# Optimization experiments

Hardware: AMD Instinct MI355X
Metric: run time of the kernel (lower is better)

The kernel has to match this reference:

```python
import jax, jax.numpy as jnp
import numpy as np
from jax import lax

B, S, D, H, T = 128, 512, 128, 128, 20


def setup_inputs() -> dict:
    key = jax.random.key(0)
    ks = jax.random.split(key, 16)
    sc = 1.0 / np.sqrt(H)
    u = lambda k, shape: jax.random.uniform(k, shape, jnp.float32, -sc, sc)
    return {
        "inputs": jax.random.normal(ks[0], (B, S, D), jnp.float32),
        "tags": jax.random.randint(ks[1], (B, S), 0, T),
        "mask": jnp.ones((B, S), jnp.bool_),
        "w_ih_f": u(ks[2], (4 * H, D)),
        "w_hh_f": u(ks[3], (4 * H, H)),
        "b_f": u(ks[4], (4 * H,)),
        "w_ih_b": u(ks[5], (4 * H, D)),
        "w_hh_b": u(ks[6], (4 * H, H)),
        "b_b": u(ks[7], (4 * H,)),
        "w_out": u(ks[8], (T, 2 * H)),
        "b_out": u(ks[9], (T,)),
        "start_trans": jax.random.uniform(ks[10], (T,), jnp.float32, -0.1, 0.1),
        "end_trans": jax.random.uniform(ks[11], (T,), jnp.float32, -0.1, 0.1),
        "trans": jax.random.uniform(ks[12], (T, T), jnp.float32, -0.1, 0.1),
    }


def _lstm_dir(x, w_ih, w_hh, b, reverse):
    # x: [B,S,D] -> hidden states [B,S,H]
    xp = jnp.einsum('bsd,gd->bsg', x, w_ih) + b  # precomputed input gates [B,S,4H]
    if reverse:
        xp = xp[:, ::-1]
    h0 = jnp.zeros((x.shape[0], H), x.dtype)
    c0 = jnp.zeros((x.shape[0], H), x.dtype)

    def step(carry, xt):
        h, c = carry
        g = xt + h @ w_hh.T
        i, f, gg, o = jnp.split(g, 4, axis=-1)
        i, f, o = jax.nn.sigmoid(i), jax.nn.sigmoid(f), jax.nn.sigmoid(o)
        c = f * c + i * jnp.tanh(gg)
        h = o * jnp.tanh(c)
        return (h, c), h

    _, hs = lax.scan(step, (h0, c0), xp.transpose(1, 0, 2))
    hs = hs.transpose(1, 0, 2)  # [B,S,H]
    if reverse:
        hs = hs[:, ::-1]
    return hs


def _crf_nll(em, tags, mask, start_trans, end_trans, trans):
    # em: [B,S,T]; torchcrf log-likelihood, reduction='mean', negated
    b, s, t = em.shape
    maskf = mask.astype(em.dtype)
    batch = jnp.arange(b)
    # numerator: score of the gold path
    num = start_trans[tags[:, 0]] + em[batch, 0, tags[:, 0]]
    em_tag = jnp.take_along_axis(em, tags[:, :, None], axis=2)[:, :, 0]  # [B,S]
    trans_tag = trans[tags[:, :-1], tags[:, 1:]]  # [B,S-1]
    num = num + jnp.sum((trans_tag + em_tag[:, 1:]) * maskf[:, 1:], axis=1)
    seq_ends = jnp.sum(mask.astype(jnp.int32), axis=1) - 1
    num = num + end_trans[tags[batch, seq_ends]]
    # denominator: forward algorithm (logsumexp semiring) via scan
    score0 = start_trans[None, :] + em[:, 0]  # [B,T]

    def step(score, inp):
        em_t, m_t = inp
        nxt = jax.nn.logsumexp(score[:, :, None] + trans[None] + em_t[:, None, :], axis=1)
        return jnp.where(m_t[:, None], nxt, score), None

    score, _ = lax.scan(step, score0, (em[:, 1:].transpose(1, 0, 2), mask[:, 1:].T))
    den = jax.nn.logsumexp(score + end_trans[None, :], axis=1)
    return -jnp.mean(num - den)


def reference(inputs, tags, mask, w_ih_f, w_hh_f, b_f, w_ih_b, w_hh_b, b_b,
              w_out, b_out, start_trans, end_trans, trans):
    h_f = _lstm_dir(inputs, w_ih_f, w_hh_f, b_f, reverse=False)
    h_b = _lstm_dir(inputs, w_ih_b, w_hh_b, b_b, reverse=True)
    lstm_out = jnp.concatenate([h_f, h_b], axis=-1)  # [B,S,2H]
    emissions = jnp.einsum('bsh,th->bst', lstm_out, w_out) + b_out  # [B,S,T]
    return _crf_nll(emissions, tags, mask, start_trans, end_trans, trans)
```

## Files before the change

### kernel.cpp

```cpp
#include <hip/hip_runtime.h>
#include <cstdint>
#include <cstddef>

#define DEVINL __device__ __forceinline__

constexpr int Bz = 128, Sl = 512, Dm = 128, Hd = 128, NC = 1024, Tt = 20;
constexpr int Mrows = Bz * Sl;

constexpr size_t OFF_WBF  = 0;
constexpr size_t OFF_HS   = 151261184;
constexpr size_t OFF_EM   = 184815616;
constexpr size_t OFF_PART = 190058496;

constexpr float LOG2E  = 1.4426950408889634f;
constexpr float LOG2E2 = 2.8853900817779268f;

DEVINL unsigned short f2bf(float f) {
    uint32_t u = __float_as_uint(f);
    u += 0x7fffu + ((u >> 16) & 1u);
    return (unsigned short)(u >> 16);
}
DEVINL float bf2f(unsigned short h) { return __uint_as_float(((uint32_t)h) << 16); }

DEVINL float rcpf(float x) { return __builtin_amdgcn_rcpf(x); }
DEVINL float exp2f_fast(float x) { return __builtin_amdgcn_exp2f(x); }

DEVINL void barrier_lds_only() {
    __asm__ __volatile__("s_waitcnt lgkmcnt(0)" ::: "memory");
    __builtin_amdgcn_s_barrier();
    __asm__ __volatile__("" ::: "memory");
}

typedef __attribute__((ext_vector_type(8))) __bf16 bf16x8;
typedef __attribute__((ext_vector_type(4))) float f32x4;
typedef _Float16 __attribute__((ext_vector_type(2))) half2_t;
typedef _Float16 __attribute__((ext_vector_type(8))) half8_t;

__global__ __launch_bounds__(256) void wcvt_k(
    const float* __restrict__ wf, const float* __restrict__ wb,
    unsigned short* __restrict__ o)
{
    const int idx = (blockIdx.x * 256 + threadIdx.x) * 4;
    const float* src = (idx < 65536) ? (wf + idx) : (wb + (idx - 65536));
    float4 v = *(const float4*)src;
    ushort4 u; u.x = f2bf(v.x); u.y = f2bf(v.y); u.z = f2bf(v.z); u.w = f2bf(v.w);
    *(ushort4*)(o + idx) = u;
}

__global__ __launch_bounds__(512, 1) void lstm_k(
    const float* __restrict__ X, const unsigned short* __restrict__ wbf,
    const float* __restrict__ b_f, const float* __restrict__ b_b,
    const float* __restrict__ whf, const float* __restrict__ whb,
    unsigned short* __restrict__ hs)
{
    __shared__ __align__(16) unsigned short xl[512 * 72];
    __shared__ __align__(16) unsigned short Xs[64 * 132];
    __shared__ __align__(16) _Float16 h_buf[2][128];
    const int dir = blockIdx.x >> 7;
    const int b   = blockIdx.x & 127;
    const int tid = threadIdx.x;
    const int lane = tid & 63;
    const int wv   = tid >> 6;
    const int ln   = lane & 15;
    const int qd   = lane >> 4;
    const int u    = wv * 16 + ln;

    const float* wsrc = dir ? whb : whf;
    half8_t wfr[4][4];
    #pragma unroll
    for (int j = 0; j < 4; ++j) {
        const float sc = (j == 2) ? LOG2E2 : LOG2E;
        const float* wrow = wsrc + (size_t)(j * 128 + u) * 128;
        #pragma unroll
        for (int kk = 0; kk < 4; ++kk) {
            float4 v0 = *(const float4*)(wrow + kk * 32 + qd * 8);
            float4 v1 = *(const float4*)(wrow + kk * 32 + qd * 8 + 4);
            half8_t hv;
            hv[0] = (_Float16)(v0.x * sc); hv[1] = (_Float16)(v0.y * sc);
            hv[2] = (_Float16)(v0.z * sc); hv[3] = (_Float16)(v0.w * sc);
            hv[4] = (_Float16)(v1.x * sc); hv[5] = (_Float16)(v1.y * sc);
            hv[6] = (_Float16)(v1.z * sc); hv[7] = (_Float16)(v1.w * sc);
            wfr[j][kk] = hv;
        }
    }

    bf16x8 wih[4][4];
    #pragma unroll
    for (int n = 0; n < 4; ++n)
        #pragma unroll
        for (int k = 0; k < 4; ++k)
            wih[n][k] = *(const bf16x8*)&wbf[((size_t)(dir * 512 + wv * 64 + n * 16 + ln)) * 128
                                            + k * 32 + qd * 8];
    const float* bsrc = dir ? b_b : b_f;
    float bvn[4];
    #pragma unroll
    for (int n = 0; n < 4; ++n) bvn[n] = bsrc[wv * 64 + n * 16 + ln];
    const float scw = ((wv >> 1) == 2) ? LOG2E2 : LOG2E;

    if (tid < 128) { h_buf[0][tid] = (_Float16)0.f; h_buf[1][tid] = (_Float16)0.f; }
    __syncthreads();

    const float* Xb = X + (size_t)b * 512 * 128;
    const int colc = (tid & 31) * 4, rowb = tid >> 5;

    unsigned short* hptr = hs + (size_t)dir * Mrows * 128 + (size_t)b * Sl * 128 + u
                              + (dir ? (size_t)(Sl - 1) * 128 : 0);
    const int hstep = dir ? -128 : 128;

    float c = 0.f;
    const f32x4 zc = {0.f, 0.f, 0.f, 0.f};

    const int r0 = (0 * 128 + u) * 72;
    const int r1 = (1 * 128 + u) * 72;
    const int r2 = (2 * 128 + u) * 72;
    const int r3 = (3 * 128 + u) * 72;

    for (int ch = 0; ch < 8; ++ch) {
        const int tlo = dir ? (448 - 64 * ch) : (64 * ch);

        #pragma unroll
        for (int r = 0; r < 4; ++r) {
            const int row = rowb + r * 16;
            float4 av = *(const float4*)&Xb[(size_t)(tlo + row) * 128 + colc];
            ushort4 au; au.x = f2bf(av.x); au.y = f2bf(av.y); au.z = f2bf(av.z); au.w = f2bf(av.w);
            *(ushort4*)&Xs[row * 132 + colc] = au;
        }
        barrier_lds_only();

        {
            f32x4 acc[4][4];
            #pragma unroll
            for (int k = 0; k < 4; ++k) {
                const int kb = k * 32 + qd * 8;
                bf16x8 af[4];
                #pragma unroll
                for (int m = 0; m < 4; ++m)
                    af[m] = *(const bf16x8*)&Xs[(m * 16 + ln) * 132 + kb];
                #pragma unroll
                for (int m = 0; m < 4; ++m)
                    #pragma unroll
                    for (int n = 0; n < 4; ++n)
                        acc[m][n] = (k == 0)
                            ? __builtin_amdgcn_mfma_f32_16x16x32_bf16(af[m], wih[n][0], zc, 0, 0, 0)
                            : __builtin_amdgcn_mfma_f32_16x16x32_bf16(af[m], wih[n][k], acc[m][n], 0, 0, 0);
            }
            #pragma unroll
            for (int m = 0; m < 4; ++m)
                #pragma unroll
                for (int n = 0; n < 4; ++n) {
                    const int gg = wv * 64 + n * 16 + ln;
                    ushort4 o;
                    o.x = f2bf((acc[m][n][0] + bvn[n]) * scw);
                    o.y = f2bf((acc[m][n][1] + bvn[n]) * scw);
                    o.z = f2bf((acc[m][n][2] + bvn[n]) * scw);
                    o.w = f2bf((acc[m][n][3] + bvn[n]) * scw);
                    *(ushort4*)&xl[gg * 72 + m * 16 + qd * 4] = o;
                }
        }
        barrier_lds_only();

        const int tt0 = dir ? 60 : 0;
        ushort4 cur0, cur1, cur2, cur3;
        {
            ushort4 q0 = *(const ushort4*)&xl[r0 + tt0];
            ushort4 q1 = *(const ushort4*)&xl[r1 + tt0];
            ushort4 q2 = *(const ushort4*)&xl[r2 + tt0];
            ushort4 q3 = *(const ushort4*)&xl[r3 + tt0];
            cur0 = dir ? ushort4{q0.w, q0.z, q0.y, q0.x} : q0;
            cur1 = dir ? ushort4{q1.w, q1.z, q1.y, q1.x} : q1;
            cur2 = dir ? ushort4{q2.w, q2.z, q2.y, q2.x} : q2;
            cur3 = dir ? ushort4{q3.w, q3.z, q3.y, q3.x} : q3;
        }

        for (int gi = 0; gi < 16; ++gi) {
            #pragma unroll
            for (int j = 0; j < 4; ++j) {
                __asm__ __volatile__(""
                    : "+v"(wfr[j][0]), "+v"(wfr[j][1]), "+v"(wfr[j][2]), "+v"(wfr[j][3]));
            }
            int ttn = dir ? (56 - gi * 4) : (gi * 4 + 4);
            if (ttn < 0) ttn = 0;
            ushort4 n0 = *(const ushort4*)&xl[r0 + ttn];
            ushort4 n1 = *(const ushort4*)&xl[r1 + ttn];
            ushort4 n2 = *(const ushort4*)&xl[r2 + ttn];
            ushort4 n3 = *(const ushort4*)&xl[r3 + ttn];

            #pragma unroll
            for (int s = 0; s < 4; ++s) {
                const int p = s & 1;
                const half8_t* hb = (const half8_t*)&h_buf[p][0];
                half8_t a0 = hb[qd];
                half8_t a1 = hb[4 + qd];
                half8_t a2 = hb[8 + qd];
                half8_t a3 = hb[12 + qd];

                f32x4 ac0, ac1, ac2, ac3;
                ac0 = __builtin_amdgcn_mfma_f32_16x16x32_f16(a0, wfr[0][0], zc, 0, 0, 0);
                ac1 = __builtin_amdgcn_mfma_f32_16x16x32_f16(a0, wfr[1][0], zc, 0, 0, 0);
                ac2 = __builtin_amdgcn_mfma_f32_16x16x32_f16(a0, wfr[2][0], zc, 0, 0, 0);
                ac3 = __builtin_amdgcn_mfma_f32_16x16x32_f16(a0, wfr[3][0], zc, 0, 0, 0);
                ac0 = __builtin_amdgcn_mfma_f32_16x16x32_f16(a1, wfr[0][1], ac0, 0, 0, 0);
                ac1 = __builtin_amdgcn_mfma_f32_16x16x32_f16(a1, wfr[1][1], ac1, 0, 0, 0);
                ac2 = __builtin_amdgcn_mfma_f32_16x16x32_f16(a1, wfr[2][1], ac2, 0, 0, 0);
                ac3 = __builtin_amdgcn_mfma_f32_16x16x32_f16(a1, wfr[3][1], ac3, 0, 0, 0);
                ac0 = __builtin_amdgcn_mfma_f32_16x16x32_f16(a2, wfr[0][2], ac0, 0, 0, 0);
                ac1 = __builtin_amdgcn_mfma_f32_16x16x32_f16(a2, wfr[1][2], ac1, 0, 0, 0);
                ac2 = __builtin_amdgcn_mfma_f32_16x16x32_f16(a2, wfr[2][2], ac2, 0, 0, 0);
                ac3 = __builtin_amdgcn_mfma_f32_16x16x32_f16(a2, wfr[3][2], ac3, 0, 0, 0);
                ac0 = __builtin_amdgcn_mfma_f32_16x16x32_f16(a3, wfr[0][3], ac0, 0, 0, 0);
                ac1 = __builtin_amdgcn_mfma_f32_16x16x32_f16(a3, wfr[1][3], ac1, 0, 0, 0);
                ac2 = __builtin_amdgcn_mfma_f32_16x16x32_f16(a3, wfr[2][3], ac2, 0, 0, 0);
                ac3 = __builtin_amdgcn_mfma_f32_16x16x32_f16(a3, wfr[3][3], ac3, 0, 0, 0);

                const unsigned short xb0 = (s == 0) ? cur0.x : (s == 1) ? cur0.y : (s == 2) ? cur0.z : cur0.w;
                const unsigned short xb1 = (s == 0) ? cur1.x : (s == 1) ? cur1.y : (s == 2) ? cur1.z : cur1.w;
                const unsigned short xb2 = (s == 0) ? cur2.x : (s == 1) ? cur2.y : (s == 2) ? cur2.z : cur2.w;
                const unsigned short xb3 = (s == 0) ? cur3.x : (s == 1) ? cur3.y : (s == 2) ? cur3.z : cur3.w;

                float t0 = ac0[0] + bf2f(xb0);
                float t1 = ac1[0] + bf2f(xb1);
                float t2 = ac2[0] + bf2f(xb2);
                float t3 = ac3[0] + bf2f(xb3);

                float gi_ = rcpf(1.f + exp2f_fast(-t0));
                float gf_ = rcpf(1.f + exp2f_fast(-t1));
                float gg_ = 2.f * rcpf(1.f + exp2f_fast(-t2)) - 1.f;
                float go_ = rcpf(1.f + exp2f_fast(-t3));
                c = fmaf(gf_, c, gi_ * gg_);
                float th = 1.f - 2.f * rcpf(1.f + exp2f_fast(LOG2E2 * c));
                float h = go_ * th;

                if (qd == 0) {
                    _Float16 hh = (_Float16)h;
                    h_buf[1 - p][u] = hh;
                    unsigned short hbits; __builtin_memcpy(&hbits, &hh, 2);
                    *hptr = hbits;
                }
                hptr += hstep;
                barrier_lds_only();
            }
            cur0 = dir ? ushort4{n0.w, n0.z, n0.y, n0.x} : n0;
            cur1 = dir ? ushort4{n1.w, n1.z, n1.y, n1.x} : n1;
            cur2 = dir ? ushort4{n2.w, n2.z, n2.y, n2.x} : n2;
            cur3 = dir ? ushort4{n3.w, n3.z, n3.y, n3.x} : n3;
        }
    }
}

__global__ __launch_bounds__(320, 1) void emis_k(
    const unsigned short* __restrict__ hs, const float* __restrict__ wout,
    const float* __restrict__ bout, float* __restrict__ em)
{
    __shared__ __align__(16) half2_t wlds[20 * 128];
    const int b  = blockIdx.x >> 2;
    const int qt = blockIdx.x & 3;
    const int tid = threadIdx.x;

    #pragma unroll
    for (int k = 0; k < 8; ++k) {
        int i = tid + k * 320;
        wlds[i] = half2_t{(_Float16)wout[2 * i], (_Float16)wout[2 * i + 1]};
    }
    __syncthreads();

    const int tag  = tid % 20;
    const int copy = tid / 20;
    half2_t wreg[128];
    {
        const uint4* wl4 = (const uint4*)&wlds[tag * 128];
        #pragma unroll
        for (int k = 0; k < 32; ++k) {
            uint4 v = wl4[k];
            __builtin_memcpy(&wreg[4 * k], &v, 16);
        }
    }
    const float bo = bout[tag];
    const unsigned short* hf_base = hs + (size_t)b * Sl * 128;
    const unsigned short* hb_base = hs + (size_t)Mrows * 128 + (size_t)b * Sl * 128;

    #pragma unroll
    for (int i = 0; i < 8; ++i) {
        const int t = qt * 128 + copy + 16 * i;
        const uint4* hf4 = (const uint4*)(hf_base + (size_t)t * 128);
        const uint4* hb4 = (const uint4*)(hb_base + (size_t)t * 128);
        float a0 = bo, a1 = 0.f, a2 = 0.f, a3 = 0.f;
        #pragma unroll
        for (int k = 0; k < 16; ++k) {
            uint4 v = hf4[k];
            half2_t h2[4]; __builtin_memcpy(h2, &v, 16);
            a0 = __builtin_amdgcn_fdot2(wreg[4 * k + 0], h2[0], a0, false);
            a1 = __builtin_amdgcn_fdot2(wreg[4 * k + 1], h2[1], a1, false);
            a2 = __builtin_amdgcn_fdot2(wreg[4 * k + 2], h2[2], a2, false);
            a3 = __builtin_amdgcn_fdot2(wreg[4 * k + 3], h2[3], a3, false);
        }
        #pragma unroll
        for (int k = 0; k < 16; ++k) {
            uint4 v = hb4[k];
            half2_t h2[4]; __builtin_memcpy(h2, &v, 16);
            a0 = __builtin_amdgcn_fdot2(wreg[64 + 4 * k + 0], h2[0], a0, false);
            a1 = __builtin_amdgcn_fdot2(wreg[64 + 4 * k + 1], h2[1], a1, false);
            a2 = __builtin_amdgcn_fdot2(wreg[64 + 4 * k + 2], h2[2], a2, false);
            a3 = __builtin_amdgcn_fdot2(wreg[64 + 4 * k + 3], h2[3], a3, false);
        }
        em[((size_t)b * Sl + t) * Tt + tag] = (a0 + a1) + (a2 + a3);
    }
}

__global__ __launch_bounds__(64) void crf_k(
    const float* __restrict__ em, const int* __restrict__ tags,
    const float* __restrict__ st, const float* __restrict__ et,
    const float* __restrict__ trans, float* __restrict__ part)
{
    const int b = blockIdx.x, lane = threadIdx.x;
    const float* emb = em + (size_t)b * Sl * Tt;
    const int* tg = tags + (size_t)b * Sl;

    float nacc = 0.f;
    for (int t = 1 + lane; t < Sl; t += 64) {
        int tp = tg[t - 1], tc = tg[t];
        nacc += trans[tp * Tt + tc] + emb[t * Tt + tc];
    }
    #pragma unroll
    for (int off = 32; off; off >>= 1) nacc += __shfl_down(nacc, off);

    float Etr[20];
    #pragma unroll
    for (int i = 0; i < 20; ++i)
        Etr[i] = (lane < 20) ? __expf(trans[i * Tt + lane]) : 0.f;

    float C = 0.f;
    float p = (lane < 20) ? __expf(st[lane] + emb[lane]) : 0.f;

    float evr[8];
    #pragma unroll
    for (int s = 0; s < 8; ++s) {
        int tt = 1 + s; tt = tt < Sl ? tt : Sl - 1;
        evr[s] = (lane < 20) ? emb[(size_t)tt * Tt + lane] : 0.f;
    }

    for (int t0 = 1; t0 < Sl; t0 += 8) {
        #pragma unroll
        for (int s = 0; s < 8; ++s) {
            const int t = t0 + s;
            if (t < Sl) {
                float ev = evr[s];
                int tf = t + 8; tf = tf < Sl ? tf : Sl - 1;
                evr[s] = (lane < 20) ? emb[(size_t)tf * Tt + lane] : 0.f;

                float q0 = 0.f, q1 = 0.f, q2 = 0.f, q3 = 0.f;
                #pragma unroll
                for (int i = 0; i < 20; i += 4) {
                    q0 = fmaf(__int_as_float(__builtin_amdgcn_readlane(__float_as_int(p), i + 0)), Etr[i + 0], q0);
                    q1 = fmaf(__int_as_float(__builtin_amdgcn_readlane(__float_as_int(p), i + 1)), Etr[i + 1], q1);
                    q2 = fmaf(__int_as_float(__builtin_amdgcn_readlane(__float_as_int(p), i + 2)), Etr[i + 2], q2);
                    q3 = fmaf(__int_as_float(__builtin_amdgcn_readlane(__float_as_int(p), i + 3)), Etr[i + 3], q3);
                }
                p = ((q0 + q1) + (q2 + q3)) * __expf(ev);
                if ((s & 3) == 3) {
                    float S0 = 0.f, S1 = 0.f, S2 = 0.f, S3 = 0.f;
                    #pragma unroll
                    for (int i = 0; i < 20; i += 4) {
                        S0 += __int_as_float(__builtin_amdgcn_readlane(__float_as_int(p), i + 0));
                        S1 += __int_as_float(__builtin_amdgcn_readlane(__float_as_int(p), i + 1));
                        S2 += __int_as_float(__builtin_amdgcn_readlane(__float_as_int(p), i + 2));
                        S3 += __int_as_float(__builtin_amdgcn_readlane(__float_as_int(p), i + 3));
                    }
                    float Ssum = (S0 + S1) + (S2 + S3);
                    C += __logf(Ssum);
                    p *= rcpf(Ssum);
                }
            }
        }
    }
    float f = (lane < 20) ? p * __expf(et[lane]) : 0.f;
    float S0 = 0.f, S1 = 0.f, S2 = 0.f, S3 = 0.f;
    #pragma unroll
    for (int i = 0; i < 20; i += 4) {
        S0 += __int_as_float(__builtin_amdgcn_readlane(__float_as_int(f), i + 0));
        S1 += __int_as_float(__builtin_amdgcn_readlane(__float_as_int(f), i + 1));
        S2 += __int_as_float(__builtin_amdgcn_readlane(__float_as_int(f), i + 2));
        S3 += __int_as_float(__builtin_amdgcn_readlane(__float_as_int(f), i + 3));
    }
    float den = C + __logf((S0 + S1) + (S2 + S3));
    if (lane == 0)
        part[b] = nacc + st[tg[0]] + emb[tg[0]] + et[tg[Sl - 1]] - den;
}

__global__ void fin_k(const float* __restrict__ part, float* __restrict__ out) {
    int l = threadIdx.x;
    float v = part[l] + part[l + 64];
    #pragma unroll
    for (int off = 32; off; off >>= 1) v += __shfl_xor(v, off);
    if (l == 0) out[0] = -v * (1.f / 128.f);
}

extern "C" void kernel_launch(void* const* d_in, const int* in_sizes, int n_in,
                              void* d_out, int out_size, void* d_ws, size_t ws_size,
                              hipStream_t stream) {
    const float* x      = (const float*)d_in[0];
    const int*   tags   = (const int*)d_in[1];
    const float* w_ih_f = (const float*)d_in[3];
    const float* w_hh_f = (const float*)d_in[4];
    const float* b_f    = (const float*)d_in[5];
    const float* w_ih_b = (const float*)d_in[6];
    const float* w_hh_b = (const float*)d_in[7];
    const float* b_b    = (const float*)d_in[8];
    const float* w_out  = (const float*)d_in[9];
    const float* b_out  = (const float*)d_in[10];
    const float* st     = (const float*)d_in[11];
    const float* et     = (const float*)d_in[12];
    const float* trans  = (const float*)d_in[13];
    float* out = (float*)d_out;

    char* ws = (char*)d_ws;
    unsigned short* wbf  = (unsigned short*)(ws + OFF_WBF);
    unsigned short* hs   = (unsigned short*)(ws + OFF_HS);
    float*          em   = (float*)(ws + OFF_EM);
    float*          part = (float*)(ws + OFF_PART);

    wcvt_k<<<128, 256, 0, stream>>>(w_ih_f, w_ih_b, wbf);
    lstm_k<<<256, 512, 0, stream>>>(x, wbf, b_f, b_b, w_hh_f, w_hh_b, hs);
    emis_k<<<Bz * 4, 320, 0, stream>>>(hs, w_out, b_out, em);
    crf_k<<<Bz, 64, 0, stream>>>(em, tags, st, et, trans, part);
    fin_k<<<1, 64, 0, stream>>>(part, out);
}
```

Before: 472.4 us.

## Overlap next chunk's input-gate GEMM with the LSTM recurrence via double-buffered LDS

The input-projection GEMM for the next 64-step chunk is split into 16 slices, one per group of 4 recurrent steps, and written into a second LDS buffer. The X load for the next chunk is issued before the recurrence starts. This hides the per-chunk GEMM and barrier stall behind the latency-bound serial recurrence. The cost is doubled xl LDS (row stride reduced from 72 to 68 to fit) and extra register pressure inside the recurrent loop.

```diff
diff --git a/kernel.cpp b/kernel.cpp
--- a/kernel.cpp
+++ b/kernel.cpp
@@ -14,6 +14,8 @@
 
 constexpr float LOG2E  = 1.4426950408889634f;
 constexpr float LOG2E2 = 2.8853900817779268f;
+
+constexpr int XLS = 68;
 
 DEVINL unsigned short f2bf(float f) {
     uint32_t u = __float_as_uint(f);
@@ -53,7 +55,7 @@
     const float* __restrict__ whf, const float* __restrict__ whb,
     unsigned short* __restrict__ hs)
 {
-    __shared__ __align__(16) unsigned short xl[512 * 72];
+    __shared__ __align__(16) unsigned short xl[2][512 * XLS];
     __shared__ __align__(16) unsigned short Xs[64 * 132];
     __shared__ __align__(16) _Float16 h_buf[2][128];
     const int dir = blockIdx.x >> 7;
@@ -110,14 +112,13 @@
     float c = 0.f;
     const f32x4 zc = {0.f, 0.f, 0.f, 0.f};
 
-    const int r0 = (0 * 128 + u) * 72;
-    const int r1 = (1 * 128 + u) * 72;
-    const int r2 = (2 * 128 + u) * 72;
-    const int r3 = (3 * 128 + u) * 72;
-
-    for (int ch = 0; ch < 8; ++ch) {
-        const int tlo = dir ? (448 - 64 * ch) : (64 * ch);
-
+    const int r0 = (0 * 128 + u) * XLS;
+    const int r1 = (1 * 128 + u) * XLS;
+    const int r2 = (2 * 128 + u) * XLS;
+    const int r3 = (3 * 128 + u) * XLS;
+
+    {
+        const int tlo = dir ? 448 : 0;
         #pragma unroll
         for (int r = 0; r < 4; ++r) {
             const int row = rowb + r * 16;
@@ -126,46 +127,60 @@
             *(ushort4*)&Xs[row * 132 + colc] = au;
         }
         barrier_lds_only();
-
-        {
-            f32x4 acc[4][4];
-            #pragma unroll
-            for (int k = 0; k < 4; ++k) {
-                const int kb = k * 32 + qd * 8;
-                bf16x8 af[4];
-                #pragma unroll
-                for (int m = 0; m < 4; ++m)
-                    af[m] = *(const bf16x8*)&Xs[(m * 16 + ln) * 132 + kb];
-                #pragma unroll
-                for (int m = 0; m < 4; ++m)
-                    #pragma unroll
-                    for (int n = 0; n < 4; ++n)
-                        acc[m][n] = (k == 0)
-                            ? __builtin_amdgcn_mfma_f32_16x16x32_bf16(af[m], wih[n][0], zc, 0, 0, 0)
-                            : __builtin_amdgcn_mfma_f32_16x16x32_bf16(af[m], wih[n][k], acc[m][n], 0, 0, 0);
-            }
+        f32x4 acc[4][4];
+        #pragma unroll
+        for (int k = 0; k < 4; ++k) {
+            const int kb = k * 32 + qd * 8;
+            bf16x8 af[4];
+            #pragma unroll
+            for (int m = 0; m < 4; ++m)
+                af[m] = *(const bf16x8*)&Xs[(m * 16 + ln) * 132 + kb];
             #pragma unroll
             for (int m = 0; m < 4; ++m)
                 #pragma unroll
-                for (int n = 0; n < 4; ++n) {
-                    const int gg = wv * 64 + n * 16 + ln;
-                    ushort4 o;
-                    o.x = f2bf((acc[m][n][0] + bvn[n]) * scw);
-                    o.y = f2bf((acc[m][n][1] + bvn[n]) * scw);
-                    o.z = f2bf((acc[m][n][2] + bvn[n]) * scw);
-                    o.w = f2bf((acc[m][n][3] + bvn[n]) * scw);
-                    *(ushort4*)&xl[gg * 72 + m * 16 + qd * 4] = o;
-                }
+                for (int n = 0; n < 4; ++n)
+                    acc[m][n] = (k == 0)
+                        ? __builtin_amdgcn_mfma_f32_16x16x32_bf16(af[m], wih[n][0], zc, 0, 0, 0)
+                        : __builtin_amdgcn_mfma_f32_16x16x32_bf16(af[m], wih[n][k], acc[m][n], 0, 0, 0);
+        }
+        #pragma unroll
+        for (int m = 0; m < 4; ++m)
+            #pragma unroll
+            for (int n = 0; n < 4; ++n) {
+                const int gg = wv * 64 + n * 16 + ln;
+                ushort4 o;
+                o.x = f2bf((acc[m][n][0] + bvn[n]) * scw);
+                o.y = f2bf((acc[m][n][1] + bvn[n]) * scw);
+                o.z = f2bf((acc[m][n][2] + bvn[n]) * scw);
+                o.w = f2bf((acc[m][n][3] + bvn[n]) * scw);
+                *(ushort4*)&xl[0][gg * XLS + m * 16 + qd * 4] = o;
+            }
+    }
+
+    int cur = 0;
+    for (int ch = 0; ch < 8; ++ch) {
+        if (ch < 7) {
+            const int tlo = dir ? (448 - 64 * (ch + 1)) : (64 * (ch + 1));
+            #pragma unroll
+            for (int r = 0; r < 4; ++r) {
+                const int row = rowb + r * 16;
+                float4 av = *(const float4*)&Xb[(size_t)(tlo + row) * 128 + colc];
+                ushort4 au; au.x = f2bf(av.x); au.y = f2bf(av.y); au.z = f2bf(av.z); au.w = f2bf(av.w);
+                *(ushort4*)&Xs[row * 132 + colc] = au;
+            }
         }
         barrier_lds_only();
+
+        const unsigned short* xb = &xl[cur][0];
+        unsigned short* xn = &xl[cur ^ 1][0];
 
         const int tt0 = dir ? 60 : 0;
         ushort4 cur0, cur1, cur2, cur3;
         {
-            ushort4 q0 = *(const ushort4*)&xl[r0 + tt0];
-            ushort4 q1 = *(const ushort4*)&xl[r1 + tt0];
-            ushort4 q2 = *(const ushort4*)&xl[r2 + tt0];
-            ushort4 q3 = *(const ushort4*)&xl[r3 + tt0];
+            ushort4 q0 = *(const ushort4*)&xb[r0 + tt0];
+            ushort4 q1 = *(const ushort4*)&xb[r1 + tt0];
+            ushort4 q2 = *(const ushort4*)&xb[r2 + tt0];
+            ushort4 q3 = *(const ushort4*)&xb[r3 + tt0];
             cur0 = dir ? ushort4{q0.w, q0.z, q0.y, q0.x} : q0;
             cur1 = dir ? ushort4{q1.w, q1.z, q1.y, q1.x} : q1;
             cur2 = dir ? ushort4{q2.w, q2.z, q2.y, q2.x} : q2;
@@ -178,12 +193,34 @@
                 __asm__ __volatile__(""
                     : "+v"(wfr[j][0]), "+v"(wfr[j][1]), "+v"(wfr[j][2]), "+v"(wfr[j][3]));
             }
+
+            if (ch < 7) {
+                const int m = gi >> 2, n = gi & 3;
+                const int kb0 = qd * 8;
+                bf16x8 af0 = *(const bf16x8*)&Xs[(m * 16 + ln) * 132 + kb0];
+                bf16x8 af1 = *(const bf16x8*)&Xs[(m * 16 + ln) * 132 + kb0 + 32];
+                bf16x8 af2 = *(const bf16x8*)&Xs[(m * 16 + ln) * 132 + kb0 + 64];
+                bf16x8 af3 = *(const bf16x8*)&Xs[(m * 16 + ln) * 132 + kb0 + 96];
+                f32x4 ga;
+                ga = __builtin_amdgcn_mfma_f32_16x16x32_bf16(af0, wih[n][0], zc, 0, 0, 0);
+                ga = __builtin_amdgcn_mfma_f32_16x16x32_bf16(af1, wih[n][1], ga, 0, 0, 0);
+                ga = __builtin_amdgcn_mfma_f32_16x16x32_bf16(af2, wih[n][2], ga, 0, 0, 0);
+                ga = __builtin_amdgcn_mfma_f32_16x16x32_bf16(af3, wih[n][3], ga, 0, 0, 0);
+                const int gg = wv * 64 + n * 16 + ln;
+                ushort4 o;
+                o.x = f2bf((ga[0] + bvn[n]) * scw);
+                o.y = f2bf((ga[1] + bvn[n]) * scw);
+                o.z = f2bf((ga[2] + bvn[n]) * scw);
+                o.w = f2bf((ga[3] + bvn[n]) * scw);
+                *(ushort4*)&xn[gg * XLS + m * 16 + qd * 4] = o;
+            }
+
             int ttn = dir ? (56 - gi * 4) : (gi * 4 + 4);
             if (ttn < 0) ttn = 0;
-            ushort4 n0 = *(const ushort4*)&xl[r0 + ttn];
-            ushort4 n1 = *(const ushort4*)&xl[r1 + ttn];
-            ushort4 n2 = *(const ushort4*)&xl[r2 + ttn];
-            ushort4 n3 = *(const ushort4*)&xl[r3 + ttn];
+            ushort4 n0 = *(const ushort4*)&xb[r0 + ttn];
+            ushort4 n1 = *(const ushort4*)&xb[r1 + ttn];
+            ushort4 n2 = *(const ushort4*)&xb[r2 + ttn];
+            ushort4 n3 = *(const ushort4*)&xb[r3 + ttn];
 
             #pragma unroll
             for (int s = 0; s < 4; ++s) {
@@ -244,6 +281,7 @@
             cur2 = dir ? ushort4{n2.w, n2.z, n2.y, n2.x} : n2;
             cur3 = dir ? ushort4{n3.w, n3.z, n3.y, n3.x} : n3;
         }
+        cur ^= 1;
     }
 }
 
```

Result: slower. 568.5 us (+20.4%).
